# Kernel tuning notes

Measured on AMD Instinct MI355X. Metric: run time of the kernel, lower is better.

The kernel has to match this reference:

```python
import jax, jax.numpy as jnp
import numpy as np


def setup_inputs() -> dict:
    key = jax.random.key(0)
    k1, k2, k3, k4 = jax.random.split(key, 4)
    B, N, F, H, C = 16, 4096, 8, 64, 256
    x = jax.random.normal(k1, (B, N, F, H), dtype=jnp.float32)
    W = jax.random.normal(k2, (H, 1), dtype=jnp.float32) / jnp.sqrt(jnp.float32(H))
    b = jax.random.normal(k3, (1,), dtype=jnp.float32) * 0.01
    segment_ids = jax.random.randint(k4, (N,), 0, C)
    return {"x": x, "W": W, "b": b, "segment_ids": segment_ids, "num_coarse": C}


def reference(x, W, b, segment_ids, num_coarse):
    # x: [B, N, F, H]; segment_ids: [N] -> coarse index; output: [B, C, F, H]
    B, N, Fdim, H = x.shape
    seg = segment_ids
    # node scores: Linear(hidden_dim, 1) on mean over feature axis -> [B, N]
    scores = (jnp.einsum('bnfh,ho->bn', x, W) / jnp.float32(Fdim)) + b[0]
    # numerically-stable per-segment softmax over fine nodes within each coarse group
    seg_max = jax.vmap(lambda s: jax.ops.segment_max(s, seg, num_segments=num_coarse))(scores)  # [B, C]
    e = jnp.exp(scores - seg_max[:, seg])                                                        # [B, N]
    denom = jax.vmap(lambda ee: jax.ops.segment_sum(ee, seg, num_segments=num_coarse))(e)        # [B, C]
    w = e / denom[:, seg]                                                                        # [B, N]
    # score-weighted segmented sum of fine features into coarse nodes
    pooled = jax.vmap(
        lambda wb, xb: jax.ops.segment_sum(wb[:, None, None] * xb, seg, num_segments=num_coarse)
    )(w, x)  # [B, C, F, H]
    return pooled
```

## Files before the change

kernel.cpp:

```cpp
#include <hip/hip_runtime.h>

#define B_ 16
#define N_ 4096
#define F_ 8
#define H_ 64
#define C_ 256
#define FH 512
#define CAP 256

__device__ __forceinline__ float dot4(const float4 a, const float4 w) {
    return (a.x * w.x + a.y * w.y) + (a.z * w.z + a.w * w.w);
}

__global__ __launch_bounds__(256, 6) void fused_pool_kernel(
    const float* __restrict__ x, const float* __restrict__ W,
    const float* __restrict__ bias, const int* __restrict__ seg,
    float* __restrict__ out)
{
    int c    = blockIdx.x & (C_ - 1);
    int b    = blockIdx.x >> 8;
    int t    = threadIdx.x;
    int wave = t >> 6;
    int lane = t & 63;
    int grp  = lane >> 5;
    int pos  = lane & 31;

    __shared__ int    list[CAP];
    __shared__ int    cnt;
    __shared__ float4 acc_sh[4][4][32];
    __shared__ float  es_sh[4];

    if (t == 0) cnt = 0;
    __syncthreads();

    const int4* seg4 = (const int4*)seg;
#pragma unroll
    for (int k = 0; k < N_ / (256 * 4); k++) {
        int i4 = t + k * 256;
        int4 s4 = seg4[i4];
        int n0 = i4 * 4;
        if (s4.x == c) { int p = atomicAdd(&cnt, 1); if (p < CAP) list[p] = n0; }
        if (s4.y == c) { int p = atomicAdd(&cnt, 1); if (p < CAP) list[p] = n0 + 1; }
        if (s4.z == c) { int p = atomicAdd(&cnt, 1); if (p < CAP) list[p] = n0 + 2; }
        if (s4.w == c) { int p = atomicAdd(&cnt, 1); if (p < CAP) list[p] = n0 + 3; }
    }
    __syncthreads();
    int m = cnt;
    if (m > CAP) m = CAP;

    float4 w4 = *(const float4*)(W + ((4 * pos) & (H_ - 1)));
    float  bb = bias[0];
    const float4* x4 = (const float4*)x;
    size_t batch_base = (size_t)b * (N_ * (FH / 4));

    float4 acc0 = {0,0,0,0}, acc1 = {0,0,0,0}, acc2 = {0,0,0,0}, acc3 = {0,0,0,0};
    float  esum = 0.0f;

    for (int base = wave * 4; base < m; base += 16) {
        int r0 = base + grp;
        int r1 = base + 2 + grp;
        int a0 = (r0 < m), a1 = (r1 < m);
        int cr0 = a0 ? r0 : (m - 1);
        int cr1 = a1 ? r1 : (m - 1);
        const float4* p0 = x4 + (batch_base + ((size_t)list[cr0] << 7) + pos);
        const float4* p1 = x4 + (batch_base + ((size_t)list[cr1] << 7) + pos);

        float4 v00, v01, v02, v03, v10, v11, v12, v13;
        if (a0) { v00 = p0[0]; v01 = p0[32]; v02 = p0[64]; v03 = p0[96]; }
        else    { v00 = v01 = v02 = v03 = make_float4(0.f, 0.f, 0.f, 0.f); }
        if (a1) { v10 = p1[0]; v11 = p1[32]; v12 = p1[64]; v13 = p1[96]; }
        else    { v10 = v11 = v12 = v13 = make_float4(0.f, 0.f, 0.f, 0.f); }

        float d0 = (dot4(v00, w4) + dot4(v01, w4)) + (dot4(v02, w4) + dot4(v03, w4));
        float d1 = (dot4(v10, w4) + dot4(v11, w4)) + (dot4(v12, w4) + dot4(v13, w4));
#pragma unroll
        for (int off = 16; off > 0; off >>= 1) {
            d0 += __shfl_xor(d0, off);
            d1 += __shfl_xor(d1, off);
        }
        float e0 = a0 ? __expf(d0 * (1.0f / F_) + bb) : 0.0f;
        float e1 = a1 ? __expf(d1 * (1.0f / F_) + bb) : 0.0f;
        esum += e0 + e1;
        acc0.x += e0 * v00.x + e1 * v10.x; acc0.y += e0 * v00.y + e1 * v10.y;
        acc0.z += e0 * v00.z + e1 * v10.z; acc0.w += e0 * v00.w + e1 * v10.w;
        acc1.x += e0 * v01.x + e1 * v11.x; acc1.y += e0 * v01.y + e1 * v11.y;
        acc1.z += e0 * v01.z + e1 * v11.z; acc1.w += e0 * v01.w + e1 * v11.w;
        acc2.x += e0 * v02.x + e1 * v12.x; acc2.y += e0 * v02.y + e1 * v12.y;
        acc2.z += e0 * v02.z + e1 * v12.z; acc2.w += e0 * v02.w + e1 * v12.w;
        acc3.x += e0 * v03.x + e1 * v13.x; acc3.y += e0 * v03.y + e1 * v13.y;
        acc3.z += e0 * v03.z + e1 * v13.z; acc3.w += e0 * v03.w + e1 * v13.w;
    }

    acc0.x += __shfl_xor(acc0.x, 32); acc0.y += __shfl_xor(acc0.y, 32);
    acc0.z += __shfl_xor(acc0.z, 32); acc0.w += __shfl_xor(acc0.w, 32);
    acc1.x += __shfl_xor(acc1.x, 32); acc1.y += __shfl_xor(acc1.y, 32);
    acc1.z += __shfl_xor(acc1.z, 32); acc1.w += __shfl_xor(acc1.w, 32);
    acc2.x += __shfl_xor(acc2.x, 32); acc2.y += __shfl_xor(acc2.y, 32);
    acc2.z += __shfl_xor(acc2.z, 32); acc2.w += __shfl_xor(acc2.w, 32);
    acc3.x += __shfl_xor(acc3.x, 32); acc3.y += __shfl_xor(acc3.y, 32);
    acc3.z += __shfl_xor(acc3.z, 32); acc3.w += __shfl_xor(acc3.w, 32);
    esum  += __shfl_xor(esum, 32);

    if (lane < 32) {
        acc_sh[wave][0][pos] = acc0;
        acc_sh[wave][1][pos] = acc1;
        acc_sh[wave][2][pos] = acc2;
        acc_sh[wave][3][pos] = acc3;
        if (lane == 0) es_sh[wave] = esum;
    }
    __syncthreads();

    if (t < 128) {
        int kk = t >> 5, pp = t & 31;
        float es  = es_sh[0] + es_sh[1] + es_sh[2] + es_sh[3];
        float inv = (m > 0) ? 1.0f / es : 0.0f;
        float4 s0 = acc_sh[0][kk][pp];
        float4 s1 = acc_sh[1][kk][pp];
        float4 s2 = acc_sh[2][kk][pp];
        float4 s3 = acc_sh[3][kk][pp];
        float4 r;
        r.x = (s0.x + s1.x + s2.x + s3.x) * inv;
        r.y = (s0.y + s1.y + s2.y + s3.y) * inv;
        r.z = (s0.z + s1.z + s2.z + s3.z) * inv;
        r.w = (s0.w + s1.w + s2.w + s3.w) * inv;
        size_t ob = ((size_t)(b * C_ + c)) * (FH / 4);
        ((float4*)out)[ob + t] = r;
    }
}

extern "C" void kernel_launch(void* const* d_in, const int* in_sizes, int n_in,
                              void* d_out, int out_size, void* d_ws, size_t ws_size,
                              hipStream_t stream)
{
    const float* x    = (const float*)d_in[0];
    const float* W    = (const float*)d_in[1];
    const float* bias = (const float*)d_in[2];
    const int*   seg  = (const int*)d_in[3];
    float* out = (float*)d_out;

    fused_pool_kernel<<<B_ * C_, 256, 0, stream>>>(x, W, bias, seg, out);
}
```

Baseline: 201.8 us.

## Precompute per-segment node lists in a separate kernel shared across batches

Moves the per-block scan of segment_ids (with shared-memory atomics) into a separate kernel that builds each segment's node list once, using wave ballots, and writes it to workspace. The pooling kernel then reads the list and count from global memory instead of rescanning all 4096 ids in every one of the B*C blocks. The scan is no longer repeated 16 times per segment, at the cost of a second launch, a dependency between kernels, and global reads of the list in the hot loop. Launch bounds also change from 6 to 4 waves per SIMD.

```diff
diff --git a/kernel.cpp b/kernel.cpp
--- a/kernel.cpp
+++ b/kernel.cpp
@@ -8,14 +8,34 @@
 #define FH 512
 #define CAP 256
 
+
+__global__ __launch_bounds__(64) void build_lists_kernel(
+    const int* __restrict__ seg, int* __restrict__ lists, int* __restrict__ cnts)
+{
+    int c    = blockIdx.x;
+    int lane = threadIdx.x;
+    int* listc = lists + c * CAP;
+    int base = 0;
+#pragma unroll 4
+    for (int k = 0; k < N_ / 64; k++) {
+        int i = k * 64 + lane;
+        bool pred = (seg[i] == c);
+        unsigned long long mask = __ballot(pred);
+        int idx = __popcll(mask & ((1ull << lane) - 1ull));
+        if (pred && (base + idx) < CAP) listc[base + idx] = i;
+        base += __popcll(mask);
+    }
+    if (lane == 0) cnts[c] = (base < CAP) ? base : CAP;
+}
+
 __device__ __forceinline__ float dot4(const float4 a, const float4 w) {
     return (a.x * w.x + a.y * w.y) + (a.z * w.z + a.w * w.w);
 }
 
-__global__ __launch_bounds__(256, 6) void fused_pool_kernel(
+__global__ __launch_bounds__(256, 4) void pool_kernel(
     const float* __restrict__ x, const float* __restrict__ W,
-    const float* __restrict__ bias, const int* __restrict__ seg,
-    float* __restrict__ out)
+    const float* __restrict__ bias, const int* __restrict__ lists,
+    const int* __restrict__ cnts, float* __restrict__ out)
 {
     int c    = blockIdx.x & (C_ - 1);
     int b    = blockIdx.x >> 8;
@@ -25,28 +45,11 @@
     int grp  = lane >> 5;
     int pos  = lane & 31;
 
-    __shared__ int    list[CAP];
-    __shared__ int    cnt;
     __shared__ float4 acc_sh[4][4][32];
     __shared__ float  es_sh[4];
 
-    if (t == 0) cnt = 0;
-    __syncthreads();
-
-    const int4* seg4 = (const int4*)seg;
-#pragma unroll
-    for (int k = 0; k < N_ / (256 * 4); k++) {
-        int i4 = t + k * 256;
-        int4 s4 = seg4[i4];
-        int n0 = i4 * 4;
-        if (s4.x == c) { int p = atomicAdd(&cnt, 1); if (p < CAP) list[p] = n0; }
-        if (s4.y == c) { int p = atomicAdd(&cnt, 1); if (p < CAP) list[p] = n0 + 1; }
-        if (s4.z == c) { int p = atomicAdd(&cnt, 1); if (p < CAP) list[p] = n0 + 2; }
-        if (s4.w == c) { int p = atomicAdd(&cnt, 1); if (p < CAP) list[p] = n0 + 3; }
-    }
-    __syncthreads();
-    int m = cnt;
-    if (m > CAP) m = CAP;
+    int m = cnts[c];
+    const int* listc = lists + c * CAP;
 
     float4 w4 = *(const float4*)(W + ((4 * pos) & (H_ - 1)));
     float  bb = bias[0];
@@ -60,10 +63,10 @@
         int r0 = base + grp;
         int r1 = base + 2 + grp;
         int a0 = (r0 < m), a1 = (r1 < m);
-        int cr0 = a0 ? r0 : (m - 1);
-        int cr1 = a1 ? r1 : (m - 1);
-        const float4* p0 = x4 + (batch_base + ((size_t)list[cr0] << 7) + pos);
-        const float4* p1 = x4 + (batch_base + ((size_t)list[cr1] << 7) + pos);
+        int n0 = listc[a0 ? r0 : 0];
+        int n1 = listc[a1 ? r1 : 0];
+        const float4* p0 = x4 + (batch_base + ((size_t)n0 << 7) + pos);
+        const float4* p1 = x4 + (batch_base + ((size_t)n1 << 7) + pos);
 
         float4 v00, v01, v02, v03, v10, v11, v12, v13;
         if (a0) { v00 = p0[0]; v01 = p0[32]; v02 = p0[64]; v03 = p0[96]; }
@@ -138,5 +141,9 @@
     const int*   seg  = (const int*)d_in[3];
     float* out = (float*)d_out;
 
-    fused_pool_kernel<<<B_ * C_, 256, 0, stream>>>(x, W, bias, seg, out);
+    int* lists = (int*)d_ws;
+    int* cnts  = lists + C_ * CAP;
+
+    build_lists_kernel<<<C_, 64, 0, stream>>>(seg, lists, cnts);
+    pool_kernel<<<B_ * C_, 256, 0, stream>>>(x, W, bias, lists, cnts, out);
 }
```

Result: slower. 223.6 us (+10.8%).

## Process two batches per block and build segment list with ballot compaction

Applied to the files above, without the earlier changes.

Each block now handles two batch indices for one coarse segment, so the segment-membership scan is done once per two batches and the grid is halved. The atomic-based list construction is replaced by a wave ballot/popcount prefix compaction, which yields deterministic, sorted node order. The batch pairing doubles the loads in flight and the register accumulators, and launch bounds drop from 6 to 4 blocks per SM to make room for them, which lowers occupancy.

```diff
diff --git a/kernel.cpp b/kernel.cpp
--- a/kernel.cpp
+++ b/kernel.cpp
@@ -12,13 +12,13 @@
     return (a.x * w.x + a.y * w.y) + (a.z * w.z + a.w * w.w);
 }
 
-__global__ __launch_bounds__(256, 6) void fused_pool_kernel(
+__global__ __launch_bounds__(256, 4) void fused_pool_kernel(
     const float* __restrict__ x, const float* __restrict__ W,
     const float* __restrict__ bias, const int* __restrict__ seg,
     float* __restrict__ out)
 {
     int c    = blockIdx.x & (C_ - 1);
-    int b    = blockIdx.x >> 8;
+    int bp   = blockIdx.x >> 8;
     int t    = threadIdx.x;
     int wave = t >> 6;
     int lane = t & 63;
@@ -26,105 +26,163 @@
     int pos  = lane & 31;
 
     __shared__ int    list[CAP];
-    __shared__ int    cnt;
-    __shared__ float4 acc_sh[4][4][32];
-    __shared__ float  es_sh[4];
-
-    if (t == 0) cnt = 0;
+    __shared__ int    wcnt[4];
+    __shared__ float4 acc_sh[2][4][4][32];
+    __shared__ float  es_sh[2][4];
+
+    int cl = 0;
+#pragma unroll
+    for (int k = 0; k < 16; k++) {
+        int i = (wave * 16 + k) * 64 + lane;
+        cl += (int)__popcll(__ballot(seg[i] == c));
+    }
+    if (lane == 0) wcnt[wave] = cl;
     __syncthreads();
-
-    const int4* seg4 = (const int4*)seg;
-#pragma unroll
-    for (int k = 0; k < N_ / (256 * 4); k++) {
-        int i4 = t + k * 256;
-        int4 s4 = seg4[i4];
-        int n0 = i4 * 4;
-        if (s4.x == c) { int p = atomicAdd(&cnt, 1); if (p < CAP) list[p] = n0; }
-        if (s4.y == c) { int p = atomicAdd(&cnt, 1); if (p < CAP) list[p] = n0 + 1; }
-        if (s4.z == c) { int p = atomicAdd(&cnt, 1); if (p < CAP) list[p] = n0 + 2; }
-        if (s4.w == c) { int p = atomicAdd(&cnt, 1); if (p < CAP) list[p] = n0 + 3; }
+    int base = 0, m = 0;
+#pragma unroll
+    for (int w2 = 0; w2 < 4; w2++) {
+        int v = wcnt[w2];
+        m += v;
+        if (w2 < wave) base += v;
+    }
+#pragma unroll
+    for (int k = 0; k < 16; k++) {
+        int i = (wave * 16 + k) * 64 + lane;
+        bool pred = (seg[i] == c);
+        unsigned long long mask = __ballot(pred);
+        int idx = (int)__popcll(mask & ((1ull << lane) - 1ull));
+        if (pred && (base + idx) < CAP) list[base + idx] = i;
+        base += (int)__popcll(mask);
     }
     __syncthreads();
-    int m = cnt;
     if (m > CAP) m = CAP;
 
     float4 w4 = *(const float4*)(W + ((4 * pos) & (H_ - 1)));
     float  bb = bias[0];
     const float4* x4 = (const float4*)x;
-    size_t batch_base = (size_t)b * (N_ * (FH / 4));
-
-    float4 acc0 = {0,0,0,0}, acc1 = {0,0,0,0}, acc2 = {0,0,0,0}, acc3 = {0,0,0,0};
-    float  esum = 0.0f;
-
-    for (int base = wave * 4; base < m; base += 16) {
-        int r0 = base + grp;
-        int r1 = base + 2 + grp;
+    size_t base0 = (size_t)(2 * bp)     * (N_ * (FH / 4));
+    size_t base1 = (size_t)(2 * bp + 1) * (N_ * (FH / 4));
+
+    float4 A0 = {0,0,0,0}, A1 = {0,0,0,0}, A2 = {0,0,0,0}, A3 = {0,0,0,0};
+    float4 B0 = {0,0,0,0}, B1 = {0,0,0,0}, B2 = {0,0,0,0}, B3 = {0,0,0,0};
+    float  es0 = 0.0f, es1 = 0.0f;
+
+    for (int rb = wave * 4; rb < m; rb += 16) {
+        int r0 = rb + grp;
+        int r1 = rb + 2 + grp;
         int a0 = (r0 < m), a1 = (r1 < m);
-        int cr0 = a0 ? r0 : (m - 1);
-        int cr1 = a1 ? r1 : (m - 1);
-        const float4* p0 = x4 + (batch_base + ((size_t)list[cr0] << 7) + pos);
-        const float4* p1 = x4 + (batch_base + ((size_t)list[cr1] << 7) + pos);
+        int n0 = list[a0 ? r0 : 0];
+        int n1 = list[a1 ? r1 : 0];
+        size_t ro0 = ((size_t)n0 << 7) + pos;
+        size_t ro1 = ((size_t)n1 << 7) + pos;
+        const float4* p0 = x4 + base0 + ro0;
+        const float4* p1 = x4 + base0 + ro1;
+        const float4* q0 = x4 + base1 + ro0;
+        const float4* q1 = x4 + base1 + ro1;
 
         float4 v00, v01, v02, v03, v10, v11, v12, v13;
-        if (a0) { v00 = p0[0]; v01 = p0[32]; v02 = p0[64]; v03 = p0[96]; }
-        else    { v00 = v01 = v02 = v03 = make_float4(0.f, 0.f, 0.f, 0.f); }
-        if (a1) { v10 = p1[0]; v11 = p1[32]; v12 = p1[64]; v13 = p1[96]; }
-        else    { v10 = v11 = v12 = v13 = make_float4(0.f, 0.f, 0.f, 0.f); }
+        float4 u00, u01, u02, u03, u10, u11, u12, u13;
+        if (a0) {
+            v00 = p0[0]; v01 = p0[32]; v02 = p0[64]; v03 = p0[96];
+            u00 = q0[0]; u01 = q0[32]; u02 = q0[64]; u03 = q0[96];
+        } else {
+            v00 = v01 = v02 = v03 = make_float4(0.f, 0.f, 0.f, 0.f);
+            u00 = u01 = u02 = u03 = make_float4(0.f, 0.f, 0.f, 0.f);
+        }
+        if (a1) {
+            v10 = p1[0]; v11 = p1[32]; v12 = p1[64]; v13 = p1[96];
+            u10 = q1[0]; u11 = q1[32]; u12 = q1[64]; u13 = q1[96];
+        } else {
+            v10 = v11 = v12 = v13 = make_float4(0.f, 0.f, 0.f, 0.f);
+            u10 = u11 = u12 = u13 = make_float4(0.f, 0.f, 0.f, 0.f);
+        }
 
         float d0 = (dot4(v00, w4) + dot4(v01, w4)) + (dot4(v02, w4) + dot4(v03, w4));
         float d1 = (dot4(v10, w4) + dot4(v11, w4)) + (dot4(v12, w4) + dot4(v13, w4));
+        float g0 = (dot4(u00, w4) + dot4(u01, w4)) + (dot4(u02, w4) + dot4(u03, w4));
+        float g1 = (dot4(u10, w4) + dot4(u11, w4)) + (dot4(u12, w4) + dot4(u13, w4));
 #pragma unroll
         for (int off = 16; off > 0; off >>= 1) {
             d0 += __shfl_xor(d0, off);
             d1 += __shfl_xor(d1, off);
+            g0 += __shfl_xor(g0, off);
+            g1 += __shfl_xor(g1, off);
         }
         float e0 = a0 ? __expf(d0 * (1.0f / F_) + bb) : 0.0f;
         float e1 = a1 ? __expf(d1 * (1.0f / F_) + bb) : 0.0f;
-        esum += e0 + e1;
-        acc0.x += e0 * v00.x + e1 * v10.x; acc0.y += e0 * v00.y + e1 * v10.y;
-        acc0.z += e0 * v00.z + e1 * v10.z; acc0.w += e0 * v00.w + e1 * v10.w;
-        acc1.x += e0 * v01.x + e1 * v11.x; acc1.y += e0 * v01.y + e1 * v11.y;
-        acc1.z += e0 * v01.z + e1 * v11.z; acc1.w += e0 * v01.w + e1 * v11.w;
-        acc2.x += e0 * v02.x + e1 * v12.x; acc2.y += e0 * v02.y + e1 * v12.y;
-        acc2.z += e0 * v02.z + e1 * v12.z; acc2.w += e0 * v02.w + e1 * v12.w;
-        acc3.x += e0 * v03.x + e1 * v13.x; acc3.y += e0 * v03.y + e1 * v13.y;
-        acc3.z += e0 * v03.z + e1 * v13.z; acc3.w += e0 * v03.w + e1 * v13.w;
-    }
-
-    acc0.x += __shfl_xor(acc0.x, 32); acc0.y += __shfl_xor(acc0.y, 32);
-    acc0.z += __shfl_xor(acc0.z, 32); acc0.w += __shfl_xor(acc0.w, 32);
-    acc1.x += __shfl_xor(acc1.x, 32); acc1.y += __shfl_xor(acc1.y, 32);
-    acc1.z += __shfl_xor(acc1.z, 32); acc1.w += __shfl_xor(acc1.w, 32);
-    acc2.x += __shfl_xor(acc2.x, 32); acc2.y += __shfl_xor(acc2.y, 32);
-    acc2.z += __shfl_xor(acc2.z, 32); acc2.w += __shfl_xor(acc2.w, 32);
-    acc3.x += __shfl_xor(acc3.x, 32); acc3.y += __shfl_xor(acc3.y, 32);
-    acc3.z += __shfl_xor(acc3.z, 32); acc3.w += __shfl_xor(acc3.w, 32);
-    esum  += __shfl_xor(esum, 32);
+        float f0 = a0 ? __expf(g0 * (1.0f / F_) + bb) : 0.0f;
+        float f1 = a1 ? __expf(g1 * (1.0f / F_) + bb) : 0.0f;
+        es0 += e0 + e1;
+        es1 += f0 + f1;
+
+        A0.x += e0 * v00.x + e1 * v10.x; A0.y += e0 * v00.y + e1 * v10.y;
+        A0.z += e0 * v00.z + e1 * v10.z; A0.w += e0 * v00.w + e1 * v10.w;
+        A1.x += e0 * v01.x + e1 * v11.x; A1.y += e0 * v01.y + e1 * v11.y;
+        A1.z += e0 * v01.z + e1 * v11.z; A1.w += e0 * v01.w + e1 * v11.w;
+        A2.x += e0 * v02.x + e1 * v12.x; A2.y += e0 * v02.y + e1 * v12.y;
+        A2.z += e0 * v02.z + e1 * v12.z; A2.w += e0 * v02.w + e1 * v12.w;
+        A3.x += e0 * v03.x + e1 * v13.x; A3.y += e0 * v03.y + e1 * v13.y;
+        A3.z += e0 * v03.z + e1 * v13.z; A3.w += e0 * v03.w + e1 * v13.w;
+
+        B0.x += f0 * u00.x + f1 * u10.x; B0.y += f0 * u00.y + f1 * u10.y;
+        B0.z += f0 * u00.z + f1 * u10.z; B0.w += f0 * u00.w + f1 * u10.w;
+        B1.x += f0 * u01.x + f1 * u11.x; B1.y += f0 * u01.y + f1 * u11.y;
+        B1.z += f0 * u01.z + f1 * u11.z; B1.w += f0 * u01.w + f1 * u11.w;
+        B2.x += f0 * u02.x + f1 * u12.x; B2.y += f0 * u02.y + f1 * u12.y;
+        B2.z += f0 * u02.z + f1 * u12.z; B2.w += f0 * u02.w + f1 * u12.w;
+        B3.x += f0 * u03.x + f1 * u13.x; B3.y += f0 * u03.y + f1 * u13.y;
+        B3.z += f0 * u03.z + f1 * u13.z; B3.w += f0 * u03.w + f1 * u13.w;
+    }
+
+    A0.x += __shfl_xor(A0.x, 32); A0.y += __shfl_xor(A0.y, 32);
+    A0.z += __shfl_xor(A0.z, 32); A0.w += __shfl_xor(A0.w, 32);
+    A1.x += __shfl_xor(A1.x, 32); A1.y += __shfl_xor(A1.y, 32);
+    A1.z += __shfl_xor(A1.z, 32); A1.w += __shfl_xor(A1.w, 32);
+    A2.x += __shfl_xor(A2.x, 32); A2.y += __shfl_xor(A2.y, 32);
+    A2.z += __shfl_xor(A2.z, 32); A2.w += __shfl_xor(A2.w, 32);
+    A3.x += __shfl_xor(A3.x, 32); A3.y += __shfl_xor(A3.y, 32);
+    A3.z += __shfl_xor(A3.z, 32); A3.w += __shfl_xor(A3.w, 32);
+    B0.x += __shfl_xor(B0.x, 32); B0.y += __shfl_xor(B0.y, 32);
+    B0.z += __shfl_xor(B0.z, 32); B0.w += __shfl_xor(B0.w, 32);
+    B1.x += __shfl_xor(B1.x, 32); B1.y += __shfl_xor(B1.y, 32);
+    B1.z += __shfl_xor(B1.z, 32); B1.w += __shfl_xor(B1.w, 32);
+    B2.x += __shfl_xor(B2.x, 32); B2.y += __shfl_xor(B2.y, 32);
+    B2.z += __shfl_xor(B2.z, 32); B2.w += __shfl_xor(B2.w, 32);
+    B3.x += __shfl_xor(B3.x, 32); B3.y += __shfl_xor(B3.y, 32);
+    B3.z += __shfl_xor(B3.z, 32); B3.w += __shfl_xor(B3.w, 32);
+    es0  += __shfl_xor(es0, 32);
+    es1  += __shfl_xor(es1, 32);
 
     if (lane < 32) {
-        acc_sh[wave][0][pos] = acc0;
-        acc_sh[wave][1][pos] = acc1;
-        acc_sh[wave][2][pos] = acc2;
-        acc_sh[wave][3][pos] = acc3;
-        if (lane == 0) es_sh[wave] = esum;
+        acc_sh[0][wave][0][pos] = A0;
+        acc_sh[0][wave][1][pos] = A1;
+        acc_sh[0][wave][2][pos] = A2;
+        acc_sh[0][wave][3][pos] = A3;
+        acc_sh[1][wave][0][pos] = B0;
+        acc_sh[1][wave][1][pos] = B1;
+        acc_sh[1][wave][2][pos] = B2;
+        acc_sh[1][wave][3][pos] = B3;
+        if (lane == 0) { es_sh[0][wave] = es0; es_sh[1][wave] = es1; }
     }
     __syncthreads();
 
-    if (t < 128) {
-        int kk = t >> 5, pp = t & 31;
-        float es  = es_sh[0] + es_sh[1] + es_sh[2] + es_sh[3];
+    {
+        int bi = t >> 7;
+        int tb = t & 127;
+        int kk = tb >> 5, pp = tb & 31;
+        float es  = es_sh[bi][0] + es_sh[bi][1] + es_sh[bi][2] + es_sh[bi][3];
         float inv = (m > 0) ? 1.0f / es : 0.0f;
-        float4 s0 = acc_sh[0][kk][pp];
-        float4 s1 = acc_sh[1][kk][pp];
-        float4 s2 = acc_sh[2][kk][pp];
-        float4 s3 = acc_sh[3][kk][pp];
+        float4 s0 = acc_sh[bi][0][kk][pp];
+        float4 s1 = acc_sh[bi][1][kk][pp];
+        float4 s2 = acc_sh[bi][2][kk][pp];
+        float4 s3 = acc_sh[bi][3][kk][pp];
         float4 r;
         r.x = (s0.x + s1.x + s2.x + s3.x) * inv;
         r.y = (s0.y + s1.y + s2.y + s3.y) * inv;
         r.z = (s0.z + s1.z + s2.z + s3.z) * inv;
         r.w = (s0.w + s1.w + s2.w + s3.w) * inv;
-        size_t ob = ((size_t)(b * C_ + c)) * (FH / 4);
-        ((float4*)out)[ob + t] = r;
+        size_t ob = ((size_t)((2 * bp + bi) * C_ + c)) * (FH / 4);
+        ((float4*)out)[ob + tb] = r;
     }
 }
 
@@ -138,5 +196,5 @@
     const int*   seg  = (const int*)d_in[3];
     float* out = (float*)d_out;
 
-    fused_pool_kernel<<<B_ * C_, 256, 0, stream>>>(x, W, bias, seg, out);
+    fused_pool_kernel<<<(B_ / 2) * C_, 256, 0, stream>>>(x, W, bias, seg, out);
 }
```

After: 202.1 us. No clear change (+0.1%).
